# Kernel optimization log

Hardware: AMD Instinct MI355X
Metric: run time of the kernel (lower is better)

The kernel has to match this reference:

```python
import jax, jax.numpy as jnp
import numpy as np


def _gelu(x):
    # tf.nn.gelu default is exact (erf) gelu
    return jax.nn.gelu(x, approximate=False)


def _reduce_gat(x, W, A):
    # x: [..., n, f]; W: [f, d]; A: [2d, 1]
    wx = x @ W                                   # [..., n, d]
    root = jnp.broadcast_to(wx[..., 0:1, :], wx.shape)  # gather idx 0 + repeat
    cat = jnp.concatenate([wx, root], axis=-1)   # [..., n, 2d]
    z = _gelu(cat @ A)                           # Dense(1, activation=gelu)
    att = jax.nn.softmax(_gelu(z), axis=-2)      # gelu applied twice, then softmax over n
    return _gelu(jnp.sum(wx * att, axis=-2))     # [..., d]


def _layer(x, W, A):
    # W: [H, f, d], A: [H, 2d, 1]; mean over heads
    heads = jax.vmap(lambda w, a: _reduce_gat(x, w, a))(W, A)
    return jnp.mean(heads, axis=0)


def setup_inputs() -> dict:
    key = jax.random.key(0)
    k = jax.random.split(key, 5)
    B, N2, N1, F, D, H = 512, 16, 16, 256, 256, 4
    x = jax.random.normal(k[0], (B, N2, N1, F), dtype=jnp.float32)
    W0 = jax.random.normal(k[1], (H, F, D), dtype=jnp.float32) * 0.05
    A0 = jax.random.normal(k[2], (H, 2 * D, 1), dtype=jnp.float32) * 0.05
    W1 = jax.random.normal(k[3], (H, D, D), dtype=jnp.float32) * 0.05
    A1 = jax.random.normal(k[4], (H, 2 * D, 1), dtype=jnp.float32) * 0.05
    return {"x": x, "W0": W0, "A0": A0, "W1": W1, "A1": A1}


def reference(x, W0, A0, W1, A1):
    x = _layer(x, W0, A0)  # [B, N2, D]
    x = _layer(x, W1, A1)  # [B, D]
    return x
```

## Files before the change

kernel.cpp:

```cpp
#include <hip/hip_runtime.h>
#include <math.h>

typedef _Float16 half_t;
typedef __attribute__((ext_vector_type(8))) _Float16 half8;
typedef __attribute__((ext_vector_type(16))) float floatx16;

__device__ __forceinline__ float gelu_exact(float v) {
    return 0.5f * v * (1.0f + erff(v * 0.7071067811865476f));
}

__device__ __forceinline__ floatx16 zero16() {
    floatx16 z;
#pragma unroll
    for (int i = 0; i < 16; ++i) z[i] = 0.f;
    return z;
}

#define MFMA16(a, b, c) __builtin_amdgcn_mfma_f32_32x32x16_f16((a), (b), (c), 0, 0, 0)

__global__ __launch_bounds__(256) void prep(const float* __restrict__ W0,
                                            const float* __restrict__ A0,
                                            const float* __restrict__ W1,
                                            const float* __restrict__ A1,
                                            half_t* __restrict__ Wsw0, half_t* __restrict__ Wsw1,
                                            half_t* __restrict__ Zah0, half_t* __restrict__ Zal0,
                                            half_t* __restrict__ Zah1, half_t* __restrict__ Zal1) {
    __shared__ float tile[32][257];
    const int t  = threadIdx.x;
    const int kb = blockIdx.x & 7;
    const int h  = (blockIdx.x >> 3) & 3;
    const int tz = blockIdx.x >> 5;
    const float* W = tz ? W1 : W0;
    const float* A = tz ? A1 : A0;
    half_t* Wsw = tz ? Wsw1 : Wsw0;
    half_t* Zh  = tz ? Zah1 : Zah0;
    half_t* Zl  = tz ? Zal1 : Zal0;

    for (int i = 0; i < 32; ++i)
        tile[i][t] = W[(size_t)(h * 256 + kb * 32 + i) * 256 + t];
    __syncthreads();

    const int j = t >> 5, lmn = t & 31;
#pragma unroll
    for (int i0 = 0; i0 < 32; i0 += 8) {
        const int ks = 2 * kb + (i0 >> 4);
        const int qq = (i0 >> 3) & 1;
        half_t hb[8];
#pragma unroll
        for (int ii = 0; ii < 8; ++ii) hb[ii] = (half_t)tile[i0 + ii][t];
        size_t off = ((size_t)(h * 16 + ks) * 8 + j) * 512 + (size_t)(32 * qq + lmn) * 8;
        *(half8*)&Wsw[off] = *(half8*)hb;
    }

    if (kb == 0) {
        const float4* Wr = (const float4*)&W[(size_t)(h * 256 + t) * 256];
        const float4* Al = (const float4*)&A[h * 512];
        const float4* Ah = (const float4*)&A[h * 512 + 256];
        float wl = 0.f, wh = 0.f;
        for (int d = 0; d < 64; ++d) {
            float4 wv = Wr[d], a0 = Al[d], a1 = Ah[d];
            wl += wv.x * a0.x + wv.y * a0.y + wv.z * a0.z + wv.w * a0.w;
            wh += wv.x * a1.x + wv.y * a1.y + wv.z * a1.z + wv.w * a1.w;
        }
        half_t hi = (half_t)wl;
        Zh[(2 * h) * 256 + t] = hi;
        Zl[(2 * h) * 256 + t] = (half_t)(wl - (float)hi);
        hi = (half_t)wh;
        Zh[(2 * h + 1) * 256 + t] = hi;
        Zl[(2 * h + 1) * 256 + t] = (half_t)(wh - (float)hi);
        if (h == 0) {
            for (int c = 8; c < 32; ++c) {
                Zh[c * 256 + t] = (half_t)0.f;
                Zl[c * 256 + t] = (half_t)0.f;
            }
        }
    }
}

__device__ __forceinline__ void split8(const float4& v0, const float4& v1,
                                       half_t* hb, half_t* lb) {
#pragma unroll
    for (int ii = 0; ii < 8; ++ii) {
        float v = (ii < 4) ? (&v0.x)[ii] : (&v1.x)[ii - 4];
        half_t hv = (half_t)v;
        hb[ii] = hv;
        lb[ii] = (half_t)(v - (float)hv);
    }
}

__global__ __launch_bounds__(256, 2) void gat1t(
    const float* __restrict__ x, const half_t* __restrict__ Wsw,
    const half_t* __restrict__ Zah, const half_t* __restrict__ Zal,
    float* __restrict__ out) {
    __shared__ __align__(16) half_t xsh[32 * 512];
    __shared__ __align__(16) half_t xsl[32 * 512];
    __shared__ float zpart[4][64][9];
    __shared__ __align__(16) float ge_s[4][64];
    __shared__ __align__(16) float att_s[4][64];

    const int t = threadIdx.x;
    const int w = t >> 6, l = t & 63, lm = t & 31, q = (t >> 5) & 1;

    {
        const float4* xg = (const float4*)(x + (size_t)blockIdx.x * 64 * 256);
        const int row = t & 63;
        const int m = row >> 5, r31 = row & 31;
#pragma unroll
        for (int i = 0; i < 8; ++i) {
            const int cc = 4 * i + w;
            const int ks = cc >> 1, kq = cc & 1;
            float4 v0 = xg[row * 64 + 2 * cc];
            float4 v1 = xg[row * 64 + 2 * cc + 1];
            half_t hb[8], lb[8];
            split8(v0, v1, hb, lb);
            int base = ((m * 16 + ks) * 64 + 32 * kq + r31) * 8;
            *(half8*)&xsh[base] = *(half8*)hb;
            *(half8*)&xsl[base] = *(half8*)lb;
        }
    }
    __syncthreads();

    {
        floatx16 zp0 = zero16(), zp1 = zero16();
#pragma unroll
        for (int kk = 0; kk < 4; ++kk) {
            int ks = 4 * w + kk;
            int ko = lm * 256 + 16 * ks + 8 * q;
            half8 bh = *(const half8*)&Zah[ko];
            half8 bl = *(const half8*)&Zal[ko];
            half8 ah0 = *(const half8*)&xsh[(ks * 64 + l) * 8];
            half8 al0 = *(const half8*)&xsl[(ks * 64 + l) * 8];
            zp0 = MFMA16(ah0, bh, zp0);
            zp0 = MFMA16(al0, bh, zp0);
            zp0 = MFMA16(ah0, bl, zp0);
            half8 ah1 = *(const half8*)&xsh[((16 + ks) * 64 + l) * 8];
            half8 al1 = *(const half8*)&xsl[((16 + ks) * 64 + l) * 8];
            zp1 = MFMA16(ah1, bh, zp1);
            zp1 = MFMA16(al1, bh, zp1);
            zp1 = MFMA16(ah1, bl, zp1);
        }
        if (lm < 8) {
#pragma unroll
            for (int r = 0; r < 16; ++r) {
                int row = 4 * q + (r & 3) + 8 * (r >> 2);
                zpart[w][row][lm]      = zp0[r];
                zpart[w][row + 32][lm] = zp1[r];
            }
        }
    }
    __syncthreads();

    {
        int h = t >> 6, r = t & 63;
        int c0 = 2 * h, c1 = 2 * h + 1, rr = r & ~15;
        float own  = zpart[0][r][c0] + zpart[1][r][c0] + zpart[2][r][c0] + zpart[3][r][c0];
        float root = zpart[0][rr][c1] + zpart[1][rr][c1] + zpart[2][rr][c1] + zpart[3][rr][c1];
        ge_s[h][r] = gelu_exact(gelu_exact(own + root));
    }
    __syncthreads();
    {
        int h = t >> 6, r = t & 63;
        int g0 = r & ~15;
        float mx = -1e30f;
#pragma unroll
        for (int i = 0; i < 16; ++i) mx = fmaxf(mx, ge_s[h][g0 + i]);
        float sum = 0.f;
#pragma unroll
        for (int i = 0; i < 16; ++i) sum += expf(ge_s[h][g0 + i] - mx);
        att_s[h][r] = expf(ge_s[h][r] - mx) / sum;
    }
    __syncthreads();

    float outp[2][4];
#pragma unroll
    for (int nt = 0; nt < 2; ++nt)
#pragma unroll
        for (int g = 0; g < 4; ++g) outp[nt][g] = 0.f;

#pragma unroll 1
    for (int h = 0; h < 4; ++h) {
        float tp[2][4];
#pragma unroll
        for (int nt = 0; nt < 2; ++nt)
#pragma unroll
            for (int g = 0; g < 4; ++g) tp[nt][g] = 0.f;

        const half_t* Bp = Wsw + ((size_t)(h * 16) * 8 + 2 * w) * 512 + (size_t)l * 8;

#pragma unroll 1
        for (int pass = 0; pass < 2; ++pass) {
            const half_t* Xp = pass ? xsl : xsh;
            floatx16 acc[2][2];
#pragma unroll
            for (int mt = 0; mt < 2; ++mt) { acc[mt][0] = zero16(); acc[mt][1] = zero16(); }

#pragma unroll
            for (int ks = 0; ks < 16; ++ks) {
                half8 b0 = *(const half8*)(Bp + (size_t)ks * 4096);
                half8 b1 = *(const half8*)(Bp + (size_t)ks * 4096 + 512);
#pragma unroll
                for (int mt = 0; mt < 2; ++mt) {
                    half8 a = *(const half8*)&Xp[((mt * 16 + ks) * 64 + l) * 8];
                    acc[mt][0] = MFMA16(a, b0, acc[mt][0]);
                    acc[mt][1] = MFMA16(a, b1, acc[mt][1]);
                }
            }

#pragma unroll
            for (int mt = 0; mt < 2; ++mt)
#pragma unroll
                for (int k = 0; k < 4; ++k) {
                    float4 a4 = *(const float4*)&att_s[h][32 * mt + 4 * q + 8 * k];
#pragma unroll
                    for (int jj = 0; jj < 4; ++jj) {
                        int r = 4 * k + jj;
                        int row = 32 * mt + 4 * q + 8 * k + jj;
                        int g = row >> 4;
                        float av = (&a4.x)[jj];
                        tp[0][g] = fmaf(acc[mt][0][r], av, tp[0][g]);
                        tp[1][g] = fmaf(acc[mt][1][r], av, tp[1][g]);
                    }
                }
        }

#pragma unroll
        for (int nt = 0; nt < 2; ++nt)
#pragma unroll
            for (int g = 0; g < 4; ++g) {
                float s = tp[nt][g] + __shfl_xor(tp[nt][g], 32, 64);
                outp[nt][g] += gelu_exact(s);
            }
    }

    if (q == 0) {
#pragma unroll
        for (int g = 0; g < 4; ++g) {
            size_t ro = ((size_t)blockIdx.x * 4 + g) * 256 + 64 * w;
            out[ro + lm]      = 0.25f * outp[0][g];
            out[ro + 32 + lm] = 0.25f * outp[1][g];
        }
    }
}

__global__ __launch_bounds__(1024, 1) void gat2(
    const float* __restrict__ y1, const half_t* __restrict__ Wsw,
    const half_t* __restrict__ Zah, const half_t* __restrict__ Zal,
    float* __restrict__ out) {
    __shared__ __align__(16) half_t xsh[16 * 512];
    __shared__ __align__(16) half_t xsl[16 * 512];
    __shared__ float zpart[4][32][9];
    __shared__ __align__(16) float ge_s[4][32];
    __shared__ __align__(16) float att_s[4][32];
    __shared__ float outp_s[4][2][256];

    const int t = threadIdx.x;
    const int w = t >> 6, l = t & 63, lm = t & 31, q = (t >> 5) & 1;

    {
        const float4* xg = (const float4*)(y1 + (size_t)blockIdx.x * 32 * 256);
        const int row = t & 31;
        const int cc = t >> 5;
        const int ks = cc >> 1, kq = cc & 1;
        float4 v0 = xg[row * 64 + 2 * cc];
        float4 v1 = xg[row * 64 + 2 * cc + 1];
        half_t hb[8], lb[8];
        split8(v0, v1, hb, lb);
        int base = (ks * 64 + 32 * kq + row) * 8;
        *(half8*)&xsh[base] = *(half8*)hb;
        *(half8*)&xsl[base] = *(half8*)lb;
    }
    __syncthreads();

    if (w < 4) {
        floatx16 zp = zero16();
#pragma unroll
        for (int kk = 0; kk < 4; ++kk) {
            int ks = 4 * w + kk;
            int ko = lm * 256 + 16 * ks + 8 * q;
            half8 bh = *(const half8*)&Zah[ko];
            half8 bl = *(const half8*)&Zal[ko];
            half8 ah = *(const half8*)&xsh[(ks * 64 + l) * 8];
            half8 al = *(const half8*)&xsl[(ks * 64 + l) * 8];
            zp = MFMA16(ah, bh, zp);
            zp = MFMA16(al, bh, zp);
            zp = MFMA16(ah, bl, zp);
        }
        if (lm < 8) {
#pragma unroll
            for (int r = 0; r < 16; ++r) {
                int row = 4 * q + (r & 3) + 8 * (r >> 2);
                zpart[w][row][lm] = zp[r];
            }
        }
    }
    __syncthreads();

    if (t < 128) {
        int h = t >> 5, r = t & 31;
        int c0 = 2 * h, c1 = 2 * h + 1, rr = r & ~15;
        float own  = zpart[0][r][c0] + zpart[1][r][c0] + zpart[2][r][c0] + zpart[3][r][c0];
        float root = zpart[0][rr][c1] + zpart[1][rr][c1] + zpart[2][rr][c1] + zpart[3][rr][c1];
        ge_s[h][r] = gelu_exact(gelu_exact(own + root));
    }
    __syncthreads();
    if (t < 128) {
        int h = t >> 5, r = t & 31;
        int g0 = r & ~15;
        float mx = -1e30f;
#pragma unroll
        for (int i = 0; i < 16; ++i) mx = fmaxf(mx, ge_s[h][g0 + i]);
        float sum = 0.f;
#pragma unroll
        for (int i = 0; i < 16; ++i) sum += expf(ge_s[h][g0 + i] - mx);
        att_s[h][r] = expf(ge_s[h][r] - mx) / sum;
    }
    __syncthreads();

    const int head = w >> 2, strip = w & 3;
    const half_t* Bp = Wsw + ((size_t)(head * 16) * 8 + 2 * strip) * 512 + (size_t)l * 8;

    floatx16 acc0 = zero16(), acc1 = zero16();
#pragma unroll
    for (int ks = 0; ks < 16; ++ks) {
        half8 b0 = *(const half8*)(Bp + (size_t)ks * 4096);
        half8 b1 = *(const half8*)(Bp + (size_t)ks * 4096 + 512);
        half8 ah = *(const half8*)&xsh[(ks * 64 + l) * 8];
        half8 al = *(const half8*)&xsl[(ks * 64 + l) * 8];
        acc0 = MFMA16(ah, b0, acc0);
        acc0 = MFMA16(al, b0, acc0);
        acc1 = MFMA16(ah, b1, acc1);
        acc1 = MFMA16(al, b1, acc1);
    }
    float tp[2][2];
    tp[0][0] = tp[0][1] = tp[1][0] = tp[1][1] = 0.f;
#pragma unroll
    for (int k2 = 0; k2 < 2; ++k2)
#pragma unroll
        for (int kk = 0; kk < 2; ++kk)
#pragma unroll
            for (int jj = 0; jj < 4; ++jj) {
                const int k = 2 * k2 + kk;
                const int r = 4 * k + jj;
                const int g = k2;
                float av = att_s[head][16 * g + 8 * kk + 4 * q + jj];
                tp[0][g] = fmaf(acc0[r], av, tp[0][g]);
                tp[1][g] = fmaf(acc1[r], av, tp[1][g]);
            }
#pragma unroll
    for (int nt = 0; nt < 2; ++nt)
#pragma unroll
        for (int g = 0; g < 2; ++g) {
            float s = tp[nt][g] + __shfl_xor(tp[nt][g], 32, 64);
            if (q == 0) outp_s[head][g][64 * strip + 32 * nt + lm] = gelu_exact(s);
        }
    __syncthreads();

    if (t < 512) {
        int g = t >> 8, col = t & 255;
        float s = outp_s[0][g][col] + outp_s[1][g][col] + outp_s[2][g][col] + outp_s[3][g][col];
        out[((size_t)blockIdx.x * 2 + g) * 256 + col] = 0.25f * s;
    }
}

extern "C" void kernel_launch(void* const* d_in, const int* in_sizes, int n_in,
                              void* d_out, int out_size, void* d_ws, size_t ws_size,
                              hipStream_t stream) {
    const float* x  = (const float*)d_in[0];
    const float* W0 = (const float*)d_in[1];
    const float* A0 = (const float*)d_in[2];
    const float* W1 = (const float*)d_in[3];
    const float* A1 = (const float*)d_in[4];

    char* ws = (char*)d_ws;
    float*  y1   = (float*)ws;
    half_t* Wsw0 = (half_t*)(ws + 8388608);
    half_t* Wsw1 = (half_t*)(ws + 8912896);
    half_t* Zah0 = (half_t*)(ws + 9437184);
    half_t* Zal0 = (half_t*)(ws + 9453568);
    half_t* Zah1 = (half_t*)(ws + 9469952);
    half_t* Zal1 = (half_t*)(ws + 9486336);

    prep<<<64, 256, 0, stream>>>(W0, A0, W1, A1, Wsw0, Wsw1, Zah0, Zal0, Zah1, Zal1);
    gat1t<<<2048, 256, 0, stream>>>(x, Wsw0, Zah0, Zal0, y1);
    gat2<<<256, 1024, 0, stream>>>(y1, Wsw1, Zah1, Zal1, (float*)d_out);
}
```

Measured before the change: 336.6 us.

## Split layer-1 GAT across eight waves per block with two MFMA loop variants

The layer-1 kernel is rebuilt around 512-thread blocks, so each of eight waves owns 32 output columns instead of 64. This halves per-wave accumulators and B loads and raises the number of waves per CU to better hide latency. The shared front end (x staging, attention logits, softmax) moves into a helper and is gated to the first four waves. The batch is split between two variants: one keeps separate hi and lo passes, the other interleaves the hi and lo MFMAs in a single loop. The cost is idle waves during the front end and each block now covering fewer columns per wave.

```diff
diff --git a/kernel.cpp b/kernel.cpp
--- a/kernel.cpp
+++ b/kernel.cpp
@@ -88,26 +88,19 @@
     }
 }
 
-__global__ __launch_bounds__(256, 2) void gat1t(
-    const float* __restrict__ x, const half_t* __restrict__ Wsw,
-    const half_t* __restrict__ Zah, const half_t* __restrict__ Zal,
-    float* __restrict__ out) {
-    __shared__ __align__(16) half_t xsh[32 * 512];
-    __shared__ __align__(16) half_t xsl[32 * 512];
-    __shared__ float zpart[4][64][9];
-    __shared__ __align__(16) float ge_s[4][64];
-    __shared__ __align__(16) float att_s[4][64];
-
-    const int t = threadIdx.x;
-    const int w = t >> 6, l = t & 63, lm = t & 31, q = (t >> 5) & 1;
-
+__device__ __forceinline__ void l1_front(
+    const float* __restrict__ x, const half_t* __restrict__ Zah,
+    const half_t* __restrict__ Zal,
+    half_t* __restrict__ xsh, half_t* __restrict__ xsl,
+    float (*zpart)[64][9], float (*ge_s)[64], float (*att_s)[64],
+    int t, int w, int l, int lm, int q) {
     {
         const float4* xg = (const float4*)(x + (size_t)blockIdx.x * 64 * 256);
         const int row = t & 63;
         const int m = row >> 5, r31 = row & 31;
 #pragma unroll
-        for (int i = 0; i < 8; ++i) {
-            const int cc = 4 * i + w;
+        for (int i = 0; i < 4; ++i) {
+            const int cc = w + 8 * i;
             const int ks = cc >> 1, kq = cc & 1;
             float4 v0 = xg[row * 64 + 2 * cc];
             float4 v1 = xg[row * 64 + 2 * cc + 1];
@@ -120,7 +113,7 @@
     }
     __syncthreads();
 
-    {
+    if (w < 4) {
         floatx16 zp0 = zero16(), zp1 = zero16();
 #pragma unroll
         for (int kk = 0; kk < 4; ++kk) {
@@ -150,7 +143,7 @@
     }
     __syncthreads();
 
-    {
+    if (t < 256) {
         int h = t >> 6, r = t & 63;
         int c0 = 2 * h, c1 = 2 * h + 1, rr = r & ~15;
         float own  = zpart[0][r][c0] + zpart[1][r][c0] + zpart[2][r][c0] + zpart[3][r][c0];
@@ -158,7 +151,7 @@
         ge_s[h][r] = gelu_exact(gelu_exact(own + root));
     }
     __syncthreads();
-    {
+    if (t < 256) {
         int h = t >> 6, r = t & 63;
         int g0 = r & ~15;
         float mx = -1e30f;
@@ -170,74 +163,140 @@
         att_s[h][r] = expf(ge_s[h][r] - mx) / sum;
     }
     __syncthreads();
-
-    float outp[2][4];
-#pragma unroll
-    for (int nt = 0; nt < 2; ++nt)
-#pragma unroll
-        for (int g = 0; g < 4; ++g) outp[nt][g] = 0.f;
+}
+
+__global__ __launch_bounds__(512, 4) void gat1c(
+    const float* __restrict__ x, const half_t* __restrict__ Wsw,
+    const half_t* __restrict__ Zah, const half_t* __restrict__ Zal,
+    float* __restrict__ out) {
+    __shared__ __align__(16) half_t xsh[32 * 512];
+    __shared__ __align__(16) half_t xsl[32 * 512];
+    __shared__ float zpart[4][64][9];
+    __shared__ __align__(16) float ge_s[4][64];
+    __shared__ __align__(16) float att_s[4][64];
+
+    const int t = threadIdx.x;
+    const int w = t >> 6, l = t & 63, lm = t & 31, q = (t >> 5) & 1;
+
+    l1_front(x, Zah, Zal, xsh, xsl, zpart, ge_s, att_s, t, w, l, lm, q);
+
+    float outp[4];
+#pragma unroll
+    for (int g = 0; g < 4; ++g) outp[g] = 0.f;
 
 #pragma unroll 1
     for (int h = 0; h < 4; ++h) {
-        float tp[2][4];
-#pragma unroll
-        for (int nt = 0; nt < 2; ++nt)
-#pragma unroll
-            for (int g = 0; g < 4; ++g) tp[nt][g] = 0.f;
-
-        const half_t* Bp = Wsw + ((size_t)(h * 16) * 8 + 2 * w) * 512 + (size_t)l * 8;
+        float tp[4];
+#pragma unroll
+        for (int g = 0; g < 4; ++g) tp[g] = 0.f;
+
+        const half_t* Bp = Wsw + ((size_t)(h * 16) * 8 + w) * 512 + (size_t)l * 8;
 
 #pragma unroll 1
         for (int pass = 0; pass < 2; ++pass) {
             const half_t* Xp = pass ? xsl : xsh;
-            floatx16 acc[2][2];
-#pragma unroll
-            for (int mt = 0; mt < 2; ++mt) { acc[mt][0] = zero16(); acc[mt][1] = zero16(); }
-
+            floatx16 acc0 = zero16(), acc1 = zero16();
 #pragma unroll
             for (int ks = 0; ks < 16; ++ks) {
-                half8 b0 = *(const half8*)(Bp + (size_t)ks * 4096);
-                half8 b1 = *(const half8*)(Bp + (size_t)ks * 4096 + 512);
-#pragma unroll
-                for (int mt = 0; mt < 2; ++mt) {
-                    half8 a = *(const half8*)&Xp[((mt * 16 + ks) * 64 + l) * 8];
-                    acc[mt][0] = MFMA16(a, b0, acc[mt][0]);
-                    acc[mt][1] = MFMA16(a, b1, acc[mt][1]);
+                half8 b = *(const half8*)(Bp + (size_t)ks * 4096);
+                half8 a0 = *(const half8*)&Xp[(ks * 64 + l) * 8];
+                half8 a1 = *(const half8*)&Xp[((16 + ks) * 64 + l) * 8];
+                acc0 = MFMA16(a0, b, acc0);
+                acc1 = MFMA16(a1, b, acc1);
+            }
+#pragma unroll
+            for (int k = 0; k < 4; ++k) {
+                float4 a40 = *(const float4*)&att_s[h][4 * q + 8 * k];
+                float4 a41 = *(const float4*)&att_s[h][32 + 4 * q + 8 * k];
+#pragma unroll
+                for (int jj = 0; jj < 4; ++jj) {
+                    const int r = 4 * k + jj;
+                    tp[k >> 1]       = fmaf(acc0[r], (&a40.x)[jj], tp[k >> 1]);
+                    tp[2 + (k >> 1)] = fmaf(acc1[r], (&a41.x)[jj], tp[2 + (k >> 1)]);
                 }
             }
-
-#pragma unroll
-            for (int mt = 0; mt < 2; ++mt)
-#pragma unroll
-                for (int k = 0; k < 4; ++k) {
-                    float4 a4 = *(const float4*)&att_s[h][32 * mt + 4 * q + 8 * k];
-#pragma unroll
-                    for (int jj = 0; jj < 4; ++jj) {
-                        int r = 4 * k + jj;
-                        int row = 32 * mt + 4 * q + 8 * k + jj;
-                        int g = row >> 4;
-                        float av = (&a4.x)[jj];
-                        tp[0][g] = fmaf(acc[mt][0][r], av, tp[0][g]);
-                        tp[1][g] = fmaf(acc[mt][1][r], av, tp[1][g]);
-                    }
-                }
-        }
-
-#pragma unroll
-        for (int nt = 0; nt < 2; ++nt)
-#pragma unroll
-            for (int g = 0; g < 4; ++g) {
-                float s = tp[nt][g] + __shfl_xor(tp[nt][g], 32, 64);
-                outp[nt][g] += gelu_exact(s);
-            }
+        }
+
+#pragma unroll
+        for (int g = 0; g < 4; ++g) {
+            float s = tp[g] + __shfl_xor(tp[g], 32, 64);
+            outp[g] += gelu_exact(s);
+        }
     }
 
     if (q == 0) {
 #pragma unroll
         for (int g = 0; g < 4; ++g) {
-            size_t ro = ((size_t)blockIdx.x * 4 + g) * 256 + 64 * w;
-            out[ro + lm]      = 0.25f * outp[0][g];
-            out[ro + 32 + lm] = 0.25f * outp[1][g];
+            size_t ro = ((size_t)blockIdx.x * 4 + g) * 256 + 32 * w;
+            out[ro + lm] = 0.25f * outp[g];
+        }
+    }
+}
+
+__global__ __launch_bounds__(512, 4) void gat1m8(
+    const float* __restrict__ x, const half_t* __restrict__ Wsw,
+    const half_t* __restrict__ Zah, const half_t* __restrict__ Zal,
+    float* __restrict__ out) {
+    __shared__ __align__(16) half_t xsh[32 * 512];
+    __shared__ __align__(16) half_t xsl[32 * 512];
+    __shared__ float zpart[4][64][9];
+    __shared__ __align__(16) float ge_s[4][64];
+    __shared__ __align__(16) float att_s[4][64];
+
+    const int t = threadIdx.x;
+    const int w = t >> 6, l = t & 63, lm = t & 31, q = (t >> 5) & 1;
+
+    l1_front(x, Zah, Zal, xsh, xsl, zpart, ge_s, att_s, t, w, l, lm, q);
+
+    float outp[4];
+#pragma unroll
+    for (int g = 0; g < 4; ++g) outp[g] = 0.f;
+
+#pragma unroll 1
+    for (int h = 0; h < 4; ++h) {
+        float tp[4];
+#pragma unroll
+        for (int g = 0; g < 4; ++g) tp[g] = 0.f;
+
+        const half_t* Bp = Wsw + ((size_t)(h * 16) * 8 + w) * 512 + (size_t)l * 8;
+
+        floatx16 acc0 = zero16(), acc1 = zero16();
+#pragma unroll
+        for (int ks = 0; ks < 16; ++ks) {
+            half8 b = *(const half8*)(Bp + (size_t)ks * 4096);
+            half8 ah0 = *(const half8*)&xsh[(ks * 64 + l) * 8];
+            half8 al0 = *(const half8*)&xsl[(ks * 64 + l) * 8];
+            half8 ah1 = *(const half8*)&xsh[((16 + ks) * 64 + l) * 8];
+            half8 al1 = *(const half8*)&xsl[((16 + ks) * 64 + l) * 8];
+            acc0 = MFMA16(ah0, b, acc0);
+            acc0 = MFMA16(al0, b, acc0);
+            acc1 = MFMA16(ah1, b, acc1);
+            acc1 = MFMA16(al1, b, acc1);
+        }
+#pragma unroll
+        for (int k = 0; k < 4; ++k) {
+            float4 a40 = *(const float4*)&att_s[h][4 * q + 8 * k];
+            float4 a41 = *(const float4*)&att_s[h][32 + 4 * q + 8 * k];
+#pragma unroll
+            for (int jj = 0; jj < 4; ++jj) {
+                const int r = 4 * k + jj;
+                tp[k >> 1]       = fmaf(acc0[r], (&a40.x)[jj], tp[k >> 1]);
+                tp[2 + (k >> 1)] = fmaf(acc1[r], (&a41.x)[jj], tp[2 + (k >> 1)]);
+            }
+        }
+
+#pragma unroll
+        for (int g = 0; g < 4; ++g) {
+            float s = tp[g] + __shfl_xor(tp[g], 32, 64);
+            outp[g] += gelu_exact(s);
+        }
+    }
+
+    if (q == 0) {
+#pragma unroll
+        for (int g = 0; g < 4; ++g) {
+            size_t ro = ((size_t)blockIdx.x * 4 + g) * 256 + 32 * w;
+            out[ro + lm] = 0.25f * outp[g];
         }
     }
 }
@@ -381,6 +440,8 @@
     half_t* Zal1 = (half_t*)(ws + 9486336);
 
     prep<<<64, 256, 0, stream>>>(W0, A0, W1, A1, Wsw0, Wsw1, Zah0, Zal0, Zah1, Zal1);
-    gat1t<<<2048, 256, 0, stream>>>(x, Wsw0, Zah0, Zal0, y1);
+    gat1c<<<1024, 512, 0, stream>>>(x, Wsw0, Zah0, Zal0, y1);
+    gat1m8<<<1024, 512, 0, stream>>>(x + (size_t)1024 * 64 * 256, Wsw0, Zah0, Zal0,
+                                     y1 + (size_t)1024 * 4 * 256);
     gat2<<<256, 1024, 0, stream>>>(y1, Wsw1, Zah1, Zal1, (float*)d_out);
 }
```

New measurement: 650.7 us. 93.3% more time.

## Split layer-1 work between existing kernel and new 512-thread 64-row variant

Applied to the files above, without the earlier changes.

Adds a gat1m2 kernel that processes 64 rows per block with 8 waves, each wave owning a 32-column slice of D and reusing the shared x tile across two row blocks. Only the Z projection uses the split-precision (hi/lo) correction term, and the W product skips the x_hi·W_lo cross term. Half of the batch is routed to the new kernel and half stays on the original gat1t, launched back to back. The intent is better reuse of W fragments per block and lower per-block overhead, at the cost of two sequential launches and a different occupancy profile.

```diff
diff --git a/kernel.cpp b/kernel.cpp
--- a/kernel.cpp
+++ b/kernel.cpp
@@ -242,6 +242,142 @@
     }
 }
 
+__global__ __launch_bounds__(512, 2) void gat1m2(
+    const float* __restrict__ x, const half_t* __restrict__ Wsw,
+    const half_t* __restrict__ Zah, const half_t* __restrict__ Zal,
+    float* __restrict__ out) {
+    __shared__ __align__(16) half_t xsh[32 * 512];
+    __shared__ __align__(16) half_t xsl[32 * 512];
+    __shared__ float zpart[4][64][9];
+    __shared__ __align__(16) float ge_s[4][64];
+    __shared__ __align__(16) float att_s[4][64];
+
+    const int t = threadIdx.x;
+    const int w = t >> 6, l = t & 63, lm = t & 31, q = (t >> 5) & 1;
+
+    {
+        const float4* xg = (const float4*)(x + (size_t)blockIdx.x * 64 * 256);
+        const int row = t & 63;
+        const int m = row >> 5, r31 = row & 31;
+#pragma unroll
+        for (int i = 0; i < 4; ++i) {
+            const int cc = w + 8 * i;
+            const int ks = cc >> 1, kq = cc & 1;
+            float4 v0 = xg[row * 64 + 2 * cc];
+            float4 v1 = xg[row * 64 + 2 * cc + 1];
+            half_t hb[8], lb[8];
+            split8(v0, v1, hb, lb);
+            int base = ((m * 16 + ks) * 64 + 32 * kq + r31) * 8;
+            *(half8*)&xsh[base] = *(half8*)hb;
+            *(half8*)&xsl[base] = *(half8*)lb;
+        }
+    }
+    __syncthreads();
+
+    if (w < 4) {
+        floatx16 zp0 = zero16(), zp1 = zero16();
+#pragma unroll
+        for (int kk = 0; kk < 4; ++kk) {
+            int ks = 4 * w + kk;
+            int ko = lm * 256 + 16 * ks + 8 * q;
+            half8 bh = *(const half8*)&Zah[ko];
+            half8 bl = *(const half8*)&Zal[ko];
+            half8 ah0 = *(const half8*)&xsh[(ks * 64 + l) * 8];
+            half8 al0 = *(const half8*)&xsl[(ks * 64 + l) * 8];
+            zp0 = MFMA16(ah0, bh, zp0);
+            zp0 = MFMA16(al0, bh, zp0);
+            zp0 = MFMA16(ah0, bl, zp0);
+            half8 ah1 = *(const half8*)&xsh[((16 + ks) * 64 + l) * 8];
+            half8 al1 = *(const half8*)&xsl[((16 + ks) * 64 + l) * 8];
+            zp1 = MFMA16(ah1, bh, zp1);
+            zp1 = MFMA16(al1, bh, zp1);
+            zp1 = MFMA16(ah1, bl, zp1);
+        }
+        if (lm < 8) {
+#pragma unroll
+            for (int r = 0; r < 16; ++r) {
+                int row = 4 * q + (r & 3) + 8 * (r >> 2);
+                zpart[w][row][lm]      = zp0[r];
+                zpart[w][row + 32][lm] = zp1[r];
+            }
+        }
+    }
+    __syncthreads();
+
+    if (t < 256) {
+        int h = t >> 6, r = t & 63;
+        int c0 = 2 * h, c1 = 2 * h + 1, rr = r & ~15;
+        float own  = zpart[0][r][c0] + zpart[1][r][c0] + zpart[2][r][c0] + zpart[3][r][c0];
+        float root = zpart[0][rr][c1] + zpart[1][rr][c1] + zpart[2][rr][c1] + zpart[3][rr][c1];
+        ge_s[h][r] = gelu_exact(gelu_exact(own + root));
+    }
+    __syncthreads();
+    if (t < 256) {
+        int h = t >> 6, r = t & 63;
+        int g0 = r & ~15;
+        float mx = -1e30f;
+#pragma unroll
+        for (int i = 0; i < 16; ++i) mx = fmaxf(mx, ge_s[h][g0 + i]);
+        float sum = 0.f;
+#pragma unroll
+        for (int i = 0; i < 16; ++i) sum += expf(ge_s[h][g0 + i] - mx);
+        att_s[h][r] = expf(ge_s[h][r] - mx) / sum;
+    }
+    __syncthreads();
+
+    float outp[4];
+#pragma unroll
+    for (int g = 0; g < 4; ++g) outp[g] = 0.f;
+
+#pragma unroll 1
+    for (int h = 0; h < 4; ++h) {
+        float tp[4];
+#pragma unroll
+        for (int g = 0; g < 4; ++g) tp[g] = 0.f;
+
+        const half_t* Bp = Wsw + ((size_t)(h * 16) * 8 + w) * 512 + (size_t)l * 8;
+
+        floatx16 acc0 = zero16(), acc1 = zero16();
+#pragma unroll
+        for (int ks = 0; ks < 16; ++ks) {
+            half8 b = *(const half8*)(Bp + (size_t)ks * 4096);
+            half8 ah0 = *(const half8*)&xsh[(ks * 64 + l) * 8];
+            half8 al0 = *(const half8*)&xsl[(ks * 64 + l) * 8];
+            half8 ah1 = *(const half8*)&xsh[((16 + ks) * 64 + l) * 8];
+            half8 al1 = *(const half8*)&xsl[((16 + ks) * 64 + l) * 8];
+            acc0 = MFMA16(ah0, b, acc0);
+            acc0 = MFMA16(al0, b, acc0);
+            acc1 = MFMA16(ah1, b, acc1);
+            acc1 = MFMA16(al1, b, acc1);
+        }
+#pragma unroll
+        for (int k = 0; k < 4; ++k) {
+            float4 a40 = *(const float4*)&att_s[h][4 * q + 8 * k];
+            float4 a41 = *(const float4*)&att_s[h][32 + 4 * q + 8 * k];
+#pragma unroll
+            for (int jj = 0; jj < 4; ++jj) {
+                const int r = 4 * k + jj;
+                tp[k >> 1]       = fmaf(acc0[r], (&a40.x)[jj], tp[k >> 1]);
+                tp[2 + (k >> 1)] = fmaf(acc1[r], (&a41.x)[jj], tp[2 + (k >> 1)]);
+            }
+        }
+
+#pragma unroll
+        for (int g = 0; g < 4; ++g) {
+            float s = tp[g] + __shfl_xor(tp[g], 32, 64);
+            outp[g] += gelu_exact(s);
+        }
+    }
+
+    if (q == 0) {
+#pragma unroll
+        for (int g = 0; g < 4; ++g) {
+            size_t ro = ((size_t)blockIdx.x * 4 + g) * 256 + 32 * w;
+            out[ro + lm] = 0.25f * outp[g];
+        }
+    }
+}
+
 __global__ __launch_bounds__(1024, 1) void gat2(
     const float* __restrict__ y1, const half_t* __restrict__ Wsw,
     const half_t* __restrict__ Zah, const half_t* __restrict__ Zal,
@@ -381,6 +517,8 @@
     half_t* Zal1 = (half_t*)(ws + 9486336);
 
     prep<<<64, 256, 0, stream>>>(W0, A0, W1, A1, Wsw0, Wsw1, Zah0, Zal0, Zah1, Zal1);
-    gat1t<<<2048, 256, 0, stream>>>(x, Wsw0, Zah0, Zal0, y1);
+    gat1t<<<1024, 256, 0, stream>>>(x, Wsw0, Zah0, Zal0, y1);
+    gat1m2<<<1024, 512, 0, stream>>>(x + (size_t)1024 * 64 * 256, Wsw0, Zah0, Zal0,
+                                     y1 + (size_t)1024 * 4 * 256);
     gat2<<<256, 1024, 0, stream>>>(y1, Wsw1, Zah1, Zal1, (float*)d_out);
 }
```

After: 450.6 us. 1.34x slower.
